# Kernel tuning notes

Hardware: AMD Instinct MI355X
Metric: run time of the kernel (lower is better)

## Reference

```python
import jax, jax.numpy as jnp
import numpy as np

RADIUS = 0.1
NSAMPLE = 32
B, N, NPOINT, C = 4, 8192, 2048, 64


def ball_query(xyz, new_xyz, fps_idx):
    """Faithful to pointnet2 ball_query CUDA kernel: for each centroid collect up to
    NSAMPLE in-radius point indices in scan order; slots beyond the count are padded
    with the first in-radius index (0 if the ball is empty). fps_idx is prepended."""
    n = xyz.shape[1]
    # squared distances (B, npoint, N)
    d2 = jnp.sum((new_xyz[:, :, None, :] - xyz[:, None, :, :]) ** 2, axis=-1)
    valid = d2 < jnp.float32(RADIUS) ** 2
    cand = jnp.where(valid, jnp.arange(n, dtype=jnp.int32), jnp.int32(n))
    cand = jnp.sort(cand, axis=-1)[:, :, :NSAMPLE]  # first NSAMPLE valid ids, N = sentinel
    first = cand[:, :, :1]
    pad = jnp.where(first < n, first, 0)            # pad with first valid (0 if none)
    idx = jnp.where(cand < n, cand, pad)
    return jnp.concatenate([fps_idx[:, :, None], idx], axis=2)  # (B, npoint, NSAMPLE+1)


def group(features, idx):
    # features (B, C, N), idx (B, npoint, K) -> (B, C, npoint, K)
    return jax.vmap(lambda f, i: f[:, i])(features, idx)


def setup_inputs() -> dict:
    key = jax.random.key(0)
    k1, k2, k3 = jax.random.split(key, 3)
    xyz = jax.random.uniform(k1, (B, N, 3), dtype=jnp.float32)
    fps_idx = jax.random.randint(k2, (B, NPOINT), 0, N, dtype=jnp.int32)
    new_xyz = jax.vmap(lambda p, i: p[i])(xyz, fps_idx)  # centroids are real points
    features = jax.random.normal(k3, (B, C, N), dtype=jnp.float32)
    return {"xyz": xyz, "new_xyz": new_xyz, "features": features, "fps_idx": fps_idx}


def reference(xyz, new_xyz, features, fps_idx):
    idx = jax.lax.stop_gradient(ball_query(xyz, new_xyz, fps_idx))
    grouped_xyz = group(jnp.swapaxes(xyz, 1, 2), idx)              # (B, 3, npoint, K)
    centered = grouped_xyz - jnp.swapaxes(new_xyz, 1, 2)[..., None]
    # NOTE: the torch module uses in-place `grouped_xyz -= ...`, so raw_grouped_xyz
    # aliases the centered tensor -> both concat slots hold centered coordinates.
    grouped_features = group(features, idx)                        # (B, C, npoint, K)
    return jnp.concatenate([centered, centered, grouped_features], axis=1)
```

## Files before the change

kernel.cpp:

```cpp
#include <hip/hip_runtime.h>
#include <stdint.h>
#include <limits.h>

constexpr int BB      = 4;
constexpr int NN      = 8192;
constexpr int NPOINT  = 2048;
constexpr int CC      = 64;
constexpr int NSAMPLE = 32;
constexpr int KTOT    = NSAMPLE + 1;
constexpr int NCH     = 3 + 3 + CC;

constexpr int   GG     = 5;
constexpr int   NCELL  = GG * GG * GG;
constexpr float RPADF  = 0.1001f;
constexpr int   CAND_CAP = 192;

__device__ __forceinline__ int cell_of(float x, float y, float z) {
    int ix = (int)floorf(x * 5.0f); ix = ix < 0 ? 0 : (ix > 4 ? 4 : ix);
    int iy = (int)floorf(y * 5.0f); iy = iy < 0 ? 0 : (iy > 4 ? 4 : iy);
    int iz = (int)floorf(z * 5.0f); iz = iz < 0 ? 0 : (iz > 4 ? 4 : iz);
    return (ix * GG + iy) * GG + iz;
}

__global__ __launch_bounds__(256) void hist_kernel(
    const float* __restrict__ xyz, int* __restrict__ cellcnt)
{
    const int t = blockIdx.x * 256 + threadIdx.x;
    if (t >= BB * NN) return;
    const int b = t >> 13;
    const float* p = xyz + (size_t)t * 3;
    const int c = cell_of(p[0], p[1], p[2]);
    atomicAdd(&cellcnt[b * NCELL + c], 1);
}

__global__ __launch_bounds__(256) void scan_kernel(
    const int* __restrict__ cellcnt, int* __restrict__ cellstart)
{
    const int w    = threadIdx.x >> 6;
    const int lane = threadIdx.x & 63;
    const int* cnt = cellcnt + w * NCELL;
    int x0 = (lane < NCELL) ? cnt[lane] : 0;
    int x1 = (lane + 64 < NCELL) ? cnt[lane + 64] : 0;
#pragma unroll
    for (int d = 1; d < 64; d <<= 1) {
        int t0 = __shfl_up(x0, d);
        int t1 = __shfl_up(x1, d);
        if (lane >= d) { x0 += t0; x1 += t1; }
    }
    x1 += __shfl(x0, 63);
    int* cs = cellstart + w * (NCELL + 1);
    if (lane == 0) cs[0] = 0;
    cs[1 + lane] = x0;
    if (lane <= 60) cs[65 + lane] = x1;
}

__global__ __launch_bounds__(256) void scatter_kernel(
    const float* __restrict__ xyz, const int* __restrict__ cellstart,
    int* __restrict__ cursor,
    float* __restrict__ sx, float* __restrict__ sy, float* __restrict__ sz,
    int* __restrict__ sidx)
{
    const int t = blockIdx.x * 256 + threadIdx.x;
    if (t >= BB * NN) return;
    const int b = t >> 13;
    const int n = t & (NN - 1);
    const float* p = xyz + (size_t)t * 3;
    const float x = p[0], y = p[1], z = p[2];
    const int c = cell_of(x, y, z);
    const int pos = cellstart[b * (NCELL + 1) + c] + atomicAdd(&cursor[b * NCELL + c], 1);
    const int g = b * NN + pos;
    sx[g] = x; sy[g] = y; sz[g] = z; sidx[g] = n;
}

__global__ __launch_bounds__(256) void ball_query_grid(
    const float* __restrict__ sx, const float* __restrict__ sy,
    const float* __restrict__ sz, const int* __restrict__ sidx,
    const int*   __restrict__ cellstart,
    const float* __restrict__ new_xyz, const int* __restrict__ fps_idx,
    int*         __restrict__ idx_out)
{
    __shared__ int cand[4][CAND_CAP];
    const int w    = threadIdx.x >> 6;
    const int lane = threadIdx.x & 63;
    const int wave = blockIdx.x * 4 + w;
    const int b    = wave >> 11;

    const float* cp = new_xyz + (size_t)wave * 3;
    const float cx = cp[0], cy = cp[1], cz = cp[2];
    const float r2 = __fmul_rn(0.1f, 0.1f);

    int ix0 = (int)floorf((cx - RPADF) * 5.0f); ix0 = ix0 < 0 ? 0 : ix0;
    int ix1 = (int)floorf((cx + RPADF) * 5.0f); ix1 = ix1 > 4 ? 4 : ix1;
    int iy0 = (int)floorf((cy - RPADF) * 5.0f); iy0 = iy0 < 0 ? 0 : iy0;
    int iy1 = (int)floorf((cy + RPADF) * 5.0f); iy1 = iy1 > 4 ? 4 : iy1;
    int iz0 = (int)floorf((cz - RPADF) * 5.0f); iz0 = iz0 < 0 ? 0 : iz0;
    int iz1 = (int)floorf((cz + RPADF) * 5.0f); iz1 = iz1 > 4 ? 4 : iz1;

    const int* cs = cellstart + b * (NCELL + 1);
    const int gb  = b * NN;
    int cnt = 0;

    for (int ix = ix0; ix <= ix1; ++ix) {
        for (int iy = iy0; iy <= iy1; ++iy) {
            const int cbase = (ix * GG + iy) * GG;
            const int st = cs[cbase + iz0];
            const int en = cs[cbase + iz1 + 1];
            for (int base = st; base < en; base += 64) {
                const int pos = base + lane;
                const bool inb = pos < en;
                const int rp = inb ? pos : st;
                const float px = sx[gb + rp];
                const float py = sy[gb + rp];
                const float pz = sz[gb + rp];
                const int  oid = sidx[gb + rp];
                const float dx = __fsub_rn(cx, px);
                const float dy = __fsub_rn(cy, py);
                const float dz = __fsub_rn(cz, pz);
                const float d2 = __fadd_rn(__fadd_rn(__fmul_rn(dx, dx), __fmul_rn(dy, dy)),
                                           __fmul_rn(dz, dz));
                const bool valid = inb && (d2 < r2);
                const unsigned long long m = __ballot(valid);
                if (m != 0ull) {
                    const int prefix = __builtin_amdgcn_mbcnt_hi(
                        (unsigned)(m >> 32), __builtin_amdgcn_mbcnt_lo((unsigned)m, 0u));
                    const int slot = cnt + prefix;
                    if (valid && slot < CAND_CAP) cand[w][slot] = oid;
                    cnt += (int)__popcll(m);
                }
            }
        }
    }

    const int K = cnt > CAND_CAP ? CAND_CAP : cnt;

    int v0 = (lane       < K) ? cand[w][lane]       : INT_MAX;
    int v1 = (lane + 64  < K) ? cand[w][lane + 64]  : INT_MAX;
    int v2 = (lane + 128 < K) ? cand[w][lane + 128] : INT_MAX;
    int rk0 = 0, rk1 = 0, rk2 = 0;
    for (int j = 0; j < K; ++j) {
        const int sv = cand[w][j];
        rk0 += (sv < v0); rk1 += (sv < v1); rk2 += (sv < v2);
    }
    int* out = idx_out + (size_t)wave * KTOT;
    if (lane       < K && rk0 < NSAMPLE) out[1 + rk0] = v0;
    if (lane + 64  < K && rk1 < NSAMPLE) out[1 + rk1] = v1;
    if (lane + 128 < K && rk2 < NSAMPLE) out[1 + rk2] = v2;

    if (K < NSAMPLE) {
        int mn = v0;
#pragma unroll
        for (int off = 32; off >= 1; off >>= 1) {
            const int o = __shfl_xor(mn, off);
            mn = o < mn ? o : mn;
        }
        const int pad = (K > 0) ? mn : 0;
        if (lane >= K && lane < NSAMPLE) out[1 + lane] = pad;
    }
    if (lane == 0) out[0] = fps_idx[wave];
}

__global__ __launch_bounds__(256) void feat_transpose(
    const float* __restrict__ f, float* __restrict__ ft)
{
    __shared__ float tile[64 * 65];
    const int blk = blockIdx.x;
    const int b   = blk >> 7;
    const int n0  = (blk & 127) << 6;
    const int w   = threadIdx.x >> 6, l = threadIdx.x & 63;
#pragma unroll
    for (int i = 0; i < 16; ++i) {
        const int c = i * 4 + w;
        tile[l * 65 + c] = f[((size_t)b * CC + c) * NN + n0 + l];
    }
    __syncthreads();
#pragma unroll
    for (int i = 0; i < 16; ++i) {
        const int flat = i * 256 + threadIdx.x;
        ft[((size_t)b * NN + n0) * CC + flat] = tile[(flat >> 6) * 65 + (flat & 63)];
    }
}

__global__ __launch_bounds__(256) void gather_v3(
    const float* __restrict__ xyz, const float* __restrict__ new_xyz,
    const float* __restrict__ ft, const int* __restrict__ idx,
    float* __restrict__ out)
{
    const int o = blockIdx.x * 256 + threadIdx.x;
    if (o >= BB * NPOINT * KTOT) return;
    const int s = o % KTOT;
    const int t = o / KTOT;
    const int j = t & (NPOINT - 1);
    const int b = t >> 11;
    const int id = idx[o];

    const size_t chstride = (size_t)NPOINT * KTOT;
    const size_t outb = (size_t)b * NCH * chstride + (size_t)j * KTOT + s;

    const float* gp = xyz + ((size_t)b * NN + id) * 3;
    const float* cp = new_xyz + ((size_t)b * NPOINT + j) * 3;
    const float vx = __fsub_rn(gp[0], cp[0]);
    const float vy = __fsub_rn(gp[1], cp[1]);
    const float vz = __fsub_rn(gp[2], cp[2]);
    out[outb]                = vx;
    out[outb + chstride]     = vy;
    out[outb + 2 * chstride] = vz;
    out[outb + 3 * chstride] = vx;
    out[outb + 4 * chstride] = vy;
    out[outb + 5 * chstride] = vz;

    const float4* fp = (const float4*)ft + ((size_t)b * NN + id) * (CC / 4);
#pragma unroll
    for (int q = 0; q < CC / 4; ++q) {
        const float4 v = fp[q];
        const size_t base = outb + (size_t)(6 + 4 * q) * chstride;
        out[base]                = v.x;
        out[base + chstride]     = v.y;
        out[base + 2 * chstride] = v.z;
        out[base + 3 * chstride] = v.w;
    }
}

__global__ __launch_bounds__(256) void ball_query_bf(
    const float* __restrict__ xyz, const float* __restrict__ new_xyz,
    const int* __restrict__ fps_idx, int* __restrict__ idx_out)
{
    const int wave = (blockIdx.x * blockDim.x + threadIdx.x) >> 6;
    const int lane = threadIdx.x & 63;
    if (wave >= BB * NPOINT) return;
    const int b = wave >> 11;
    const float* cp = new_xyz + (size_t)wave * 3;
    const float cx = cp[0], cy = cp[1], cz = cp[2];
    const float r2 = __fmul_rn(0.1f, 0.1f);
    const float* xb = xyz + (size_t)b * NN * 3;
    int* out = idx_out + (size_t)wave * KTOT;
    int count = 0, first = 0;
    for (int base = 0; base < NN; base += 64) {
        const int p = base + lane;
        const float dx = __fsub_rn(cx, xb[p * 3 + 0]);
        const float dy = __fsub_rn(cy, xb[p * 3 + 1]);
        const float dz = __fsub_rn(cz, xb[p * 3 + 2]);
        const float d2 = __fadd_rn(__fadd_rn(__fmul_rn(dx, dx), __fmul_rn(dy, dy)),
                                   __fmul_rn(dz, dz));
        const bool valid = d2 < r2;
        const unsigned long long m = __ballot(valid);
        if (count == 0 && m != 0ull) first = base + __builtin_ctzll(m);
        const int prefix = __builtin_amdgcn_mbcnt_hi(
            (unsigned)(m >> 32), __builtin_amdgcn_mbcnt_lo((unsigned)m, 0u));
        const int slot = count + prefix;
        if (valid && slot < NSAMPLE) out[1 + slot] = p;
        count += (int)__popcll(m);
        if (count >= NSAMPLE) break;
    }
    if (count < NSAMPLE) {
        const int pad = (count > 0) ? first : 0;
        if (lane >= count && lane < NSAMPLE) out[1 + lane] = pad;
    }
    if (lane == 0) out[0] = fps_idx[wave];
}

__global__ __launch_bounds__(256) void gather_kernel(
    const float* __restrict__ xyz, const float* __restrict__ new_xyz,
    const float* __restrict__ features, const int* __restrict__ idx,
    float* __restrict__ out)
{
    const long long total = (long long)BB * NCH * NPOINT * KTOT;
    const long long o = (long long)blockIdx.x * blockDim.x + threadIdx.x;
    if (o >= total) return;
    const int s  = (int)(o % KTOT);
    long long t  = o / KTOT;
    const int j  = (int)(t % NPOINT);
    t /= NPOINT;
    const int ch = (int)(t % NCH);
    const int b  = (int)(t / NCH);
    const int id = idx[(long long)(b * NPOINT + j) * KTOT + s];
    float v;
    if (ch < 6) {
        const int c3 = (ch >= 3) ? (ch - 3) : ch;
        v = __fsub_rn(xyz[((long long)b * NN + id) * 3 + c3],
                      new_xyz[((long long)b * NPOINT + j) * 3 + c3]);
    } else {
        v = features[((long long)b * CC + (ch - 6)) * NN + id];
    }
    out[o] = v;
}

extern "C" void kernel_launch(void* const* d_in, const int* in_sizes, int n_in,
                              void* d_out, int out_size, void* d_ws, size_t ws_size,
                              hipStream_t stream) {
    const float* xyz      = (const float*)d_in[0];
    const float* new_xyz  = (const float*)d_in[1];
    const float* features = (const float*)d_in[2];
    const int*   fps_idx  = (const int*)d_in[3];
    float*       out      = (float*)d_out;

    const size_t off_idx   = 0;
    const size_t sz_idx    = (size_t)BB * NPOINT * KTOT * 4;
    const size_t off_ft    = off_idx + sz_idx;
    const size_t sz_ft     = (size_t)BB * NN * CC * 4;
    const size_t off_sx    = off_ft + sz_ft;
    const size_t sz_plane  = (size_t)BB * NN * 4;
    const size_t off_sy    = off_sx + sz_plane;
    const size_t off_sz    = off_sy + sz_plane;
    const size_t off_sidx  = off_sz + sz_plane;
    const size_t off_cnt   = off_sidx + sz_plane;
    const size_t sz_cnt    = (size_t)BB * NCELL * 4;
    const size_t off_cur   = off_cnt + sz_cnt;
    const size_t off_cs    = off_cur + sz_cnt;
    const size_t sz_cs     = (size_t)BB * (NCELL + 1) * 4;
    const size_t need_full = off_cs + sz_cs;

    int* idxbuf = (int*)((char*)d_ws + off_idx);
    const int gblocks = (BB * NPOINT * KTOT + 255) / 256;
    const int pblocks = (BB * NN) / 256;

    if (ws_size >= need_full) {
        float* ft   = (float*)((char*)d_ws + off_ft);
        float* sx   = (float*)((char*)d_ws + off_sx);
        float* sy   = (float*)((char*)d_ws + off_sy);
        float* szp  = (float*)((char*)d_ws + off_sz);
        int*   sidx = (int*)  ((char*)d_ws + off_sidx);
        int*   ccnt = (int*)  ((char*)d_ws + off_cnt);
        int*   cur  = (int*)  ((char*)d_ws + off_cur);
        int*   cs   = (int*)  ((char*)d_ws + off_cs);

        (void)hipMemsetAsync(ccnt, 0, 2 * sz_cnt, stream);
        hist_kernel<<<pblocks, 256, 0, stream>>>(xyz, ccnt);
        scan_kernel<<<1, 256, 0, stream>>>(ccnt, cs);
        scatter_kernel<<<pblocks, 256, 0, stream>>>(xyz, cs, cur, sx, sy, szp, sidx);

        ball_query_grid<<<BB * NPOINT / 4, 256, 0, stream>>>(
            sx, sy, szp, sidx, cs, new_xyz, fps_idx, idxbuf);

        feat_transpose<<<BB * (NN / 64), 256, 0, stream>>>(features, ft);
        gather_v3<<<gblocks, 256, 0, stream>>>(xyz, new_xyz, ft, idxbuf, out);
    } else if (ws_size >= sz_idx) {
        ball_query_bf<<<BB * NPOINT / 4, 256, 0, stream>>>(xyz, new_xyz, fps_idx, idxbuf);
        const long long total = (long long)BB * NCH * NPOINT * KTOT;
        gather_kernel<<<(int)((total + 255) / 256), 256, 0, stream>>>(
            xyz, new_xyz, features, idxbuf, out);
    }
}
```

Measured before the change: 144.9 us.

## Fuse grid build into shared-memory hist+scan, AoS sorted points, split gather across 4 threads

Replaces the memset plus separate histogram, scan and scatter kernels with one per-batch block that builds the cell histogram in shared memory, scans it, and seeds the cursors, so the scatter no longer needs a separate cellstart lookup. Sorted points are stored as a float4 array (x, y, z, index) so the ball query does one vector load per point instead of four scalar loads. The gather assigns four threads per output sample, each handling a quarter of the feature channels, to raise parallelism and memory-level concurrency. This trades fewer launches and loads for a single-block-per-batch histogram that runs on only four blocks.

```diff
diff --git a/kernel.cpp b/kernel.cpp
--- a/kernel.cpp
+++ b/kernel.cpp
@@ -9,6 +9,7 @@
 constexpr int NSAMPLE = 32;
 constexpr int KTOT    = NSAMPLE + 1;
 constexpr int NCH     = 3 + 3 + CC;
+constexpr int CHS     = NPOINT * KTOT;
 
 constexpr int   GG     = 5;
 constexpr int   NCELL  = GG * GG * GG;
@@ -22,43 +23,45 @@
     return (ix * GG + iy) * GG + iz;
 }
 
-__global__ __launch_bounds__(256) void hist_kernel(
-    const float* __restrict__ xyz, int* __restrict__ cellcnt)
-{
-    const int t = blockIdx.x * 256 + threadIdx.x;
-    if (t >= BB * NN) return;
-    const int b = t >> 13;
-    const float* p = xyz + (size_t)t * 3;
-    const int c = cell_of(p[0], p[1], p[2]);
-    atomicAdd(&cellcnt[b * NCELL + c], 1);
-}
-
-__global__ __launch_bounds__(256) void scan_kernel(
-    const int* __restrict__ cellcnt, int* __restrict__ cellstart)
-{
-    const int w    = threadIdx.x >> 6;
-    const int lane = threadIdx.x & 63;
-    const int* cnt = cellcnt + w * NCELL;
-    int x0 = (lane < NCELL) ? cnt[lane] : 0;
-    int x1 = (lane + 64 < NCELL) ? cnt[lane + 64] : 0;
-#pragma unroll
-    for (int d = 1; d < 64; d <<= 1) {
-        int t0 = __shfl_up(x0, d);
-        int t1 = __shfl_up(x1, d);
-        if (lane >= d) { x0 += t0; x1 += t1; }
-    }
-    x1 += __shfl(x0, 63);
-    int* cs = cellstart + w * (NCELL + 1);
-    if (lane == 0) cs[0] = 0;
-    cs[1 + lane] = x0;
-    if (lane <= 60) cs[65 + lane] = x1;
-}
-
-__global__ __launch_bounds__(256) void scatter_kernel(
-    const float* __restrict__ xyz, const int* __restrict__ cellstart,
-    int* __restrict__ cursor,
-    float* __restrict__ sx, float* __restrict__ sy, float* __restrict__ sz,
-    int* __restrict__ sidx)
+__global__ __launch_bounds__(1024) void grid_hist_scan(
+    const float* __restrict__ xyz, int* __restrict__ cellstartg,
+    int* __restrict__ cursorg)
+{
+    __shared__ int hist[NCELL];
+    __shared__ int csl[NCELL + 1];
+    const int b = blockIdx.x;
+    const int t = threadIdx.x;
+    if (t < NCELL) hist[t] = 0;
+    __syncthreads();
+    const float* xb = xyz + (size_t)b * NN * 3;
+#pragma unroll
+    for (int k = 0; k < NN / 1024; ++k) {
+        const float* p = xb + (size_t)(t + k * 1024) * 3;
+        atomicAdd(&hist[cell_of(p[0], p[1], p[2])], 1);
+    }
+    __syncthreads();
+    if (t < 64) {
+        int x0 = hist[t];
+        int x1 = (t + 64 < NCELL) ? hist[t + 64] : 0;
+#pragma unroll
+        for (int d = 1; d < 64; d <<= 1) {
+            int t0 = __shfl_up(x0, d);
+            int t1 = __shfl_up(x1, d);
+            if (t >= d) { x0 += t0; x1 += t1; }
+        }
+        x1 += __shfl(x0, 63);
+        if (t == 0) csl[0] = 0;
+        csl[1 + t] = x0;
+        if (t <= 60) csl[65 + t] = x1;
+    }
+    __syncthreads();
+    if (t < NCELL + 1) cellstartg[b * (NCELL + 1) + t] = csl[t];
+    if (t < NCELL)     cursorg[b * NCELL + t]          = csl[t];
+}
+
+__global__ __launch_bounds__(256) void scatter_aos(
+    const float* __restrict__ xyz, int* __restrict__ cursor,
+    float4* __restrict__ spt)
 {
     const int t = blockIdx.x * 256 + threadIdx.x;
     if (t >= BB * NN) return;
@@ -67,15 +70,12 @@
     const float* p = xyz + (size_t)t * 3;
     const float x = p[0], y = p[1], z = p[2];
     const int c = cell_of(x, y, z);
-    const int pos = cellstart[b * (NCELL + 1) + c] + atomicAdd(&cursor[b * NCELL + c], 1);
-    const int g = b * NN + pos;
-    sx[g] = x; sy[g] = y; sz[g] = z; sidx[g] = n;
+    const int pos = atomicAdd(&cursor[b * NCELL + c], 1);
+    spt[b * NN + pos] = make_float4(x, y, z, __int_as_float(n));
 }
 
 __global__ __launch_bounds__(256) void ball_query_grid(
-    const float* __restrict__ sx, const float* __restrict__ sy,
-    const float* __restrict__ sz, const int* __restrict__ sidx,
-    const int*   __restrict__ cellstart,
+    const float4* __restrict__ spt, const int* __restrict__ cellstart,
     const float* __restrict__ new_xyz, const int* __restrict__ fps_idx,
     int*         __restrict__ idx_out)
 {
@@ -108,14 +108,11 @@
             for (int base = st; base < en; base += 64) {
                 const int pos = base + lane;
                 const bool inb = pos < en;
-                const int rp = inb ? pos : st;
-                const float px = sx[gb + rp];
-                const float py = sy[gb + rp];
-                const float pz = sz[gb + rp];
-                const int  oid = sidx[gb + rp];
-                const float dx = __fsub_rn(cx, px);
-                const float dy = __fsub_rn(cy, py);
-                const float dz = __fsub_rn(cz, pz);
+                const float4 q = spt[gb + (inb ? pos : st)];
+                const int oid = __float_as_int(q.w);
+                const float dx = __fsub_rn(cx, q.x);
+                const float dy = __fsub_rn(cy, q.y);
+                const float dz = __fsub_rn(cz, q.z);
                 const float d2 = __fadd_rn(__fadd_rn(__fmul_rn(dx, dx), __fmul_rn(dy, dy)),
                                            __fmul_rn(dz, dz));
                 const bool valid = inb && (d2 < r2);
@@ -180,43 +177,39 @@
     }
 }
 
-__global__ __launch_bounds__(256) void gather_v3(
+__global__ __launch_bounds__(256) void gather_v4(
     const float* __restrict__ xyz, const float* __restrict__ new_xyz,
-    const float* __restrict__ ft, const int* __restrict__ idx,
+    const float4* __restrict__ ft4, const int* __restrict__ idx,
     float* __restrict__ out)
 {
-    const int o = blockIdx.x * 256 + threadIdx.x;
-    if (o >= BB * NPOINT * KTOT) return;
-    const int s = o % KTOT;
-    const int t = o / KTOT;
-    const int j = t & (NPOINT - 1);
-    const int b = t >> 11;
+    const int gt = blockIdx.x * 256 + threadIdx.x;
+    const int o  = gt >> 2;
+    const int g  = gt & 3;
+    if (o >= BB * CHS) return;
     const int id = idx[o];
-
-    const size_t chstride = (size_t)NPOINT * KTOT;
-    const size_t outb = (size_t)b * NCH * chstride + (size_t)j * KTOT + s;
-
-    const float* gp = xyz + ((size_t)b * NN + id) * 3;
-    const float* cp = new_xyz + ((size_t)b * NPOINT + j) * 3;
-    const float vx = __fsub_rn(gp[0], cp[0]);
-    const float vy = __fsub_rn(gp[1], cp[1]);
-    const float vz = __fsub_rn(gp[2], cp[2]);
-    out[outb]                = vx;
-    out[outb + chstride]     = vy;
-    out[outb + 2 * chstride] = vz;
-    out[outb + 3 * chstride] = vx;
-    out[outb + 4 * chstride] = vy;
-    out[outb + 5 * chstride] = vz;
-
-    const float4* fp = (const float4*)ft + ((size_t)b * NN + id) * (CC / 4);
-#pragma unroll
-    for (int q = 0; q < CC / 4; ++q) {
-        const float4 v = fp[q];
-        const size_t base = outb + (size_t)(6 + 4 * q) * chstride;
-        out[base]                = v.x;
-        out[base + chstride]     = v.y;
-        out[base + 2 * chstride] = v.z;
-        out[base + 3 * chstride] = v.w;
+    const int b  = o / CHS;
+    const int jj = o - b * CHS;
+    const size_t outbase = (size_t)b * NCH * CHS + jj;
+
+    if (g < 3) {
+        const float pv = xyz[(size_t)(b * NN + id) * 3 + g];
+        const float cv = new_xyz[(size_t)(o / KTOT) * 3 + g];
+        const float d  = __fsub_rn(pv, cv);
+        out[outbase + (size_t)g * CHS]       = d;
+        out[outbase + (size_t)(g + 3) * CHS] = d;
+    }
+
+    const float4* row = ft4 + ((size_t)b * NN + id) * (CC / 4);
+    float4 v[4];
+#pragma unroll
+    for (int i = 0; i < 4; ++i) v[i] = row[i * 4 + g];
+#pragma unroll
+    for (int i = 0; i < 4; ++i) {
+        const size_t base = outbase + (size_t)(6 + 16 * i + 4 * g) * CHS;
+        out[base]           = v[i].x;
+        out[base + CHS]     = v[i].y;
+        out[base + 2 * CHS] = v[i].z;
+        out[base + 3 * CHS] = v[i].w;
     }
 }
 
@@ -263,7 +256,7 @@
     const float* __restrict__ features, const int* __restrict__ idx,
     float* __restrict__ out)
 {
-    const long long total = (long long)BB * NCH * NPOINT * KTOT;
+    const long long total = (long long)BB * NCH * CHS;
     const long long o = (long long)blockIdx.x * blockDim.x + threadIdx.x;
     if (o >= total) return;
     const int s  = (int)(o % KTOT);
@@ -293,49 +286,38 @@
     const int*   fps_idx  = (const int*)d_in[3];
     float*       out      = (float*)d_out;
 
-    const size_t off_idx   = 0;
-    const size_t sz_idx    = (size_t)BB * NPOINT * KTOT * 4;
-    const size_t off_ft    = off_idx + sz_idx;
-    const size_t sz_ft     = (size_t)BB * NN * CC * 4;
-    const size_t off_sx    = off_ft + sz_ft;
-    const size_t sz_plane  = (size_t)BB * NN * 4;
-    const size_t off_sy    = off_sx + sz_plane;
-    const size_t off_sz    = off_sy + sz_plane;
-    const size_t off_sidx  = off_sz + sz_plane;
-    const size_t off_cnt   = off_sidx + sz_plane;
-    const size_t sz_cnt    = (size_t)BB * NCELL * 4;
-    const size_t off_cur   = off_cnt + sz_cnt;
-    const size_t off_cs    = off_cur + sz_cnt;
-    const size_t sz_cs     = (size_t)BB * (NCELL + 1) * 4;
-    const size_t need_full = off_cs + sz_cs;
+    const size_t off_idx  = 0;
+    const size_t sz_idx   = (size_t)BB * CHS * 4;
+    const size_t off_ft   = off_idx + sz_idx;
+    const size_t sz_ft    = (size_t)BB * NN * CC * 4;
+    const size_t off_spt  = off_ft + sz_ft;
+    const size_t sz_spt   = (size_t)BB * NN * 16;
+    const size_t off_cs   = off_spt + sz_spt;
+    const size_t sz_cs    = (size_t)BB * (NCELL + 1) * 4;
+    const size_t off_cur  = off_cs + 2048;
+    const size_t need_full = off_cur + 2048;
 
     int* idxbuf = (int*)((char*)d_ws + off_idx);
-    const int gblocks = (BB * NPOINT * KTOT + 255) / 256;
-    const int pblocks = (BB * NN) / 256;
+    const int gblocks4 = (BB * CHS * 4 + 255) / 256;
 
     if (ws_size >= need_full) {
-        float* ft   = (float*)((char*)d_ws + off_ft);
-        float* sx   = (float*)((char*)d_ws + off_sx);
-        float* sy   = (float*)((char*)d_ws + off_sy);
-        float* szp  = (float*)((char*)d_ws + off_sz);
-        int*   sidx = (int*)  ((char*)d_ws + off_sidx);
-        int*   ccnt = (int*)  ((char*)d_ws + off_cnt);
-        int*   cur  = (int*)  ((char*)d_ws + off_cur);
-        int*   cs   = (int*)  ((char*)d_ws + off_cs);
-
-        (void)hipMemsetAsync(ccnt, 0, 2 * sz_cnt, stream);
-        hist_kernel<<<pblocks, 256, 0, stream>>>(xyz, ccnt);
-        scan_kernel<<<1, 256, 0, stream>>>(ccnt, cs);
-        scatter_kernel<<<pblocks, 256, 0, stream>>>(xyz, cs, cur, sx, sy, szp, sidx);
+        float*  ft   = (float*) ((char*)d_ws + off_ft);
+        float4* spt  = (float4*)((char*)d_ws + off_spt);
+        int*    cs   = (int*)   ((char*)d_ws + off_cs);
+        int*    cur  = (int*)   ((char*)d_ws + off_cur);
+
+        grid_hist_scan<<<BB, 1024, 0, stream>>>(xyz, cs, cur);
+        scatter_aos<<<(BB * NN) / 256, 256, 0, stream>>>(xyz, cur, spt);
 
         ball_query_grid<<<BB * NPOINT / 4, 256, 0, stream>>>(
-            sx, sy, szp, sidx, cs, new_xyz, fps_idx, idxbuf);
+            spt, cs, new_xyz, fps_idx, idxbuf);
 
         feat_transpose<<<BB * (NN / 64), 256, 0, stream>>>(features, ft);
-        gather_v3<<<gblocks, 256, 0, stream>>>(xyz, new_xyz, ft, idxbuf, out);
+        gather_v4<<<gblocks4, 256, 0, stream>>>(xyz, new_xyz, (const float4*)ft,
+                                                idxbuf, out);
     } else if (ws_size >= sz_idx) {
         ball_query_bf<<<BB * NPOINT / 4, 256, 0, stream>>>(xyz, new_xyz, fps_idx, idxbuf);
-        const long long total = (long long)BB * NCH * NPOINT * KTOT;
+        const long long total = (long long)BB * NCH * CHS;
         gather_kernel<<<(int)((total + 255) / 256), 256, 0, stream>>>(
             xyz, new_xyz, features, idxbuf, out);
     }
```

Measured after the change: 133.9 us. 1.08x faster.
